# Kernel optimization log

Hardware: AMD Instinct MI355X
Metric: run time of the kernel (lower is better)

## Reference

```python
import jax, jax.numpy as jnp
import numpy as np


def _local_indices(H, W, K):
    # KxK local window per pixel; border neighbors clamped to the image (replicate padding)
    half = K // 2
    d = np.arange(-half, half + 1)
    r = np.clip(np.arange(H)[:, None, None, None] + d[None, None, :, None], 0, H - 1)
    c = np.clip(np.arange(W)[None, :, None, None] + d[None, None, None, :], 0, W - 1)
    return (r * W + c).reshape(H * W, K * K).astype(np.int32)


def setup_inputs():
    B, C, H, W = 2, 32, 128, 128
    K, S = 25, 1024
    N = H * W
    k1, k2, k3, k4 = jax.random.split(jax.random.key(0), 4)
    key_feat = jax.random.normal(k1, (B, C, H, W), dtype=jnp.float32)
    query_feat = jax.random.normal(k2, (B, C, H, W), dtype=jnp.float32)
    segment_target = jax.random.randint(k3, (B, 1, H, W), 0, 64, dtype=jnp.int32)
    local = jnp.broadcast_to(jnp.asarray(_local_indices(H, W, K))[None], (B, N, K * K))
    rand_glob = jax.random.randint(k4, (B, N, S - K * K), 0, N, dtype=jnp.int32)
    sample_inds = jnp.concatenate([local, rand_glob], axis=-1)  # [B, N, S]
    return {"key_feat": key_feat, "query_feat": query_feat,
            "segment_target": segment_target, "sample_inds": sample_inds}


def _affinity_logits(key_f, query_f, sample_inds, chunk=1024):
    # key_f, query_f: [B, N, C]; sample_inds: [B, N, S]
    B, N, C = key_f.shape
    S = sample_inds.shape[-1]
    nchunks = N // chunk
    q_c = query_f.reshape(B, nchunks, chunk, C).transpose(1, 0, 2, 3)
    i_c = sample_inds.reshape(B, nchunks, chunk, S).transpose(1, 0, 2, 3)

    def body(carry, args):
        q, idx = args                                   # [B, chunk, C], [B, chunk, S]
        kg = jax.vmap(lambda kb, ib: kb[ib])(key_f, idx)  # [B, chunk, S, C]
        return carry, jnp.einsum('bnsc,bnc->bns', kg, q)

    _, lc = jax.lax.scan(body, None, (q_c, i_c))        # [nchunks, B, chunk, S]
    logits = lc.transpose(1, 0, 2, 3).reshape(B, N, S)
    return logits * (C ** -0.5)


def _loss(logits, sample_inds, segment_target):
    B, N, S = logits.shape
    seg = segment_target.reshape(B, N)
    samples = jax.vmap(lambda s, i: s[i])(seg, sample_inds)      # [B, N, S]
    targets = (seg[:, :, None] == samples).astype(logits.dtype)
    mask = (seg != 0).astype(logits.dtype)[:, :, None]           # [B, N, 1]
    # weighted_softmax(logits, mask)
    xe = jnp.exp(logits - jnp.max(logits, -1, keepdims=True))
    denom = jnp.sum(xe * mask, -1, keepdims=True)
    y_prob = xe * mask / (denom + 1e-9)
    y_pred = jnp.log(jnp.clip(y_prob, 1e-8, None))
    y_true = targets / (jnp.sum(targets, -1, keepdims=True) + 1e-9)
    # F.kl_div(y_pred, y_true, reduction='none') with 0*log(0) = 0
    kl = jnp.where(y_true > 0,
                   y_true * (jnp.log(jnp.clip(y_true, 1e-30, None)) - y_pred),
                   0.0) * mask
    agg_mask = (jnp.sum(mask, -1) > 0).astype(logits.dtype)
    return jnp.sum(kl) / (jnp.sum(agg_mask) + 1e-9)


def reference(key_feat, query_feat, segment_target, sample_inds):
    B, C, H, W = key_feat.shape
    N = H * W
    key_f = key_feat.reshape(B, C, N).transpose(0, 2, 1)    # [B, N, C]
    query_f = query_feat.reshape(B, C, N).transpose(0, 2, 1)
    logits = _affinity_logits(key_f, query_f, sample_inds)  # [B, N, S], scaled by C**-0.5
    loss = _loss(logits, sample_inds, segment_target)
    return (logits, loss)
```

## Files before the change

### kernel.cpp

```cpp
#include <hip/hip_runtime.h>
#include <stdint.h>

typedef _Float16 h2 __attribute__((ext_vector_type(2)));

static constexpr int CDIM = 32;
static constexpr int NPIX = 16384;
static constexpr int SSAM = 1024;
static constexpr int ROWS_PER_BLOCK = 16;

__device__ __forceinline__ uint16_t f2h(float f) {
    union { _Float16 h; uint16_t u; } c;
    c.h = (_Float16)f;
    return c.u;
}

template<int CTRL>
__device__ __forceinline__ float dpp_add(float x) {
    int y = __builtin_amdgcn_mov_dpp(__float_as_int(x), CTRL, 0xF, 0xF, true);
    return x + __int_as_float(y);
}

__device__ __forceinline__ float dot2(h2 a, h2 b, float c) {
    return __builtin_amdgcn_fdot2(a, b, c, false);
}

__global__ __launch_bounds__(256)
void prep_kernel(const float* __restrict__ key_f,
                 const float* __restrict__ query_f,
                 const int* __restrict__ seg32,
                 uint8_t* __restrict__ key16,
                 uint8_t* __restrict__ q16,
                 uint8_t* __restrict__ seg8,
                 int N, int rows, float scale)
{
    int gI = blockIdx.x * 256 + threadIdx.x;
    if (gI >= rows) return;
    int b = gI / N, n = gI - b * N;
    const size_t cb = (size_t)b * CDIM;

    uint32_t kp[16], qp[16];
#pragma unroll
    for (int c = 0; c < CDIM; c += 2) {
        float k0 = key_f[(cb + c) * N + n];
        float k1 = key_f[(cb + c + 1) * N + n];
        float q0 = query_f[(cb + c) * N + n] * scale;
        float q1 = query_f[(cb + c + 1) * N + n] * scale;
        kp[c >> 1] = (uint32_t)f2h(k0) | ((uint32_t)f2h(k1) << 16);
        qp[c >> 1] = (uint32_t)f2h(q0) | ((uint32_t)f2h(q1) << 16);
    }
    uint4* ko = (uint4*)(key16 + ((size_t)gI << 6));
    uint4* qo = (uint4*)(q16 + ((size_t)gI << 6));
#pragma unroll
    for (int j = 0; j < 4; ++j) {
        ko[j] = make_uint4(kp[4*j], kp[4*j+1], kp[4*j+2], kp[4*j+3]);
        qo[j] = make_uint4(qp[4*j], qp[4*j+1], qp[4*j+2], qp[4*j+3]);
    }
    seg8[gI] = (uint8_t)seg32[gI];
}

__global__ __launch_bounds__(256)
void affinity_multi(const int* __restrict__ inds,
                    const uint8_t* __restrict__ key16,
                    const uint8_t* __restrict__ q16,
                    const uint8_t* __restrict__ seg8,
                    float* __restrict__ out,
                    float* __restrict__ ws_kl)
{
    const int tid  = threadIdx.x;
    const int row0 = blockIdx.x * ROWS_PER_BLOCK;
    const int b    = row0 >> 14;
    const int lane = tid & 63;
    const int w    = tid >> 6;
    const int g    = lane >> 2;
    const int sub  = lane & 3;

    __shared__ __align__(16) uint8_t seg_lds[NPIX];
    __shared__ __align__(16) int     idx_lds[2][SSAM];
    __shared__ float red[2][3][4];

    const uint8_t* sbg = seg8 + ((size_t)b << 14);
#pragma unroll
    for (int r = 0; r < 4; ++r)
        ((uint4*)seg_lds)[(r << 8) + tid] = ((const uint4*)sbg)[(r << 8) + tid];
    ((int4*)idx_lds[0])[tid] = ((const int4*)(inds + ((size_t)row0 << 10)))[tid];
    uint4 qcur = *(const uint4*)(q16 + ((size_t)row0 << 6) + (sub << 4));
    __syncthreads();

    const uint8_t* kb = key16 + ((size_t)b << 20);
    const uint32_t subs = (uint32_t)(sub << 4);
    const int sbase = (w << 8) + g;

    for (int r = 0; r < ROWS_PER_BLOCK; ++r) {
        const int row = row0 + r;
        const int p   = r & 1;
        const int* cur = idx_lds[p];
        const bool hasNext = (r + 1 < ROWS_PER_BLOCK);

        h2 qh0, qh1, qh2, qh3;
        {
            union { uint4 u; h2 h[4]; } qc; qc.u = qcur;
            qh0 = qc.h[0]; qh1 = qc.h[1]; qh2 = qc.h[2]; qh3 = qc.h[3];
        }
        const int seg_n = (int)seg_lds[row & 0x3FFF];

        int idxs[16];
#pragma unroll
        for (int i = 0; i < 16; ++i)
            idxs[i] = cur[sbase + (i << 4)];

        uint4 kd[16];
#pragma unroll
        for (int i = 0; i < 16; ++i)
            kd[i] = *(const uint4*)(kb + (((uint32_t)idxs[i] << 6) | subs));

        int4 pre; uint4 qnext;
        if (hasNext) {
            pre   = ((const int4*)(inds + ((size_t)(row + 1) << 10)))[tid];
            qnext = *(const uint4*)(q16 + ((size_t)(row + 1) << 6) + (sub << 4));
        }
        int tfm = 0;
#pragma unroll
        for (int j = 0; j < 4; ++j) {
            int idx = cur[sbase + (((j << 2) | sub) << 4)];
            if ((int)seg_lds[idx] == seg_n) tfm |= 1 << j;
        }

        float lgo0 = 0.f, lgo1 = 0.f, lgo2 = 0.f, lgo3 = 0.f;
#pragma unroll
        for (int i = 0; i < 16; ++i) {
            union { uint4 u; h2 h[4]; } kc; kc.u = kd[i];
            float acc = dot2(kc.h[0], qh0, 0.f);
            acc = dot2(kc.h[1], qh1, acc);
            acc = dot2(kc.h[2], qh2, acc);
            acc = dot2(kc.h[3], qh3, acc);
            acc = dpp_add<0xB1>(acc);
            acc = dpp_add<0x4E>(acc);
            if (sub == (i & 3)) {
                if ((i >> 2) == 0) lgo0 = acc;
                if ((i >> 2) == 1) lgo1 = acc;
                if ((i >> 2) == 2) lgo2 = acc;
                if ((i >> 2) == 3) lgo3 = acc;
            }
        }

        const size_t rowbase = (size_t)row << 10;
        float* op = out + rowbase + (w << 8) + (sub << 4) + g;
        op[0]   = lgo0;
        op[64]  = lgo1;
        op[128] = lgo2;
        op[192] = lgo3;

        float z  = ((__expf(lgo0) + __expf(lgo1)) + (__expf(lgo2) + __expf(lgo3)));
        float tc = (float)__popc((unsigned)tfm);
        float sl = 0.f;
        sl += (tfm & 1) ? lgo0 : 0.f;
        sl += (tfm & 2) ? lgo1 : 0.f;
        sl += (tfm & 4) ? lgo2 : 0.f;
        sl += (tfm & 8) ? lgo3 : 0.f;

#pragma unroll
        for (int off = 32; off >= 1; off >>= 1) {
            z  += __shfl_xor(z,  off, 64);
            tc += __shfl_xor(tc, off, 64);
            sl += __shfl_xor(sl, off, 64);
        }
        if (lane == 0) {
            red[p][0][w] = z;
            red[p][1][w] = tc;
            red[p][2][w] = sl;
        }
        __syncthreads();

        if (tid == 0) {
            if (seg_n != 0) {
                const float Z  = (red[p][0][0] + red[p][0][1]) + (red[p][0][2] + red[p][0][3]);
                const float T  = (red[p][1][0] + red[p][1][1]) + (red[p][1][2] + red[p][1][3]);
                const float SL = (red[p][2][0] + red[p][2][1]) + (red[p][2][2] + red[p][2][3]);
                ws_kl[row] = -__logf(T) - SL / T + __logf(Z);
            } else {
                ws_kl[row] = 0.f;
            }
        }

        if (hasNext) {
            ((int4*)idx_lds[p ^ 1])[tid] = pre;
            qcur = qnext;
        }
    }
}

__global__ __launch_bounds__(256)
void affinity_fallback(const float* __restrict__ key_f,
                       const float* __restrict__ query_f,
                       const int*   __restrict__ seg32,
                       const int*   __restrict__ inds,
                       float* __restrict__ out,
                       float* __restrict__ ws_kl,
                       int N, int S, float scale)
{
    const int bid = blockIdx.x;
    const int tid = threadIdx.x;
    const int b   = bid / N;

    __shared__ float q_lds[CDIM];
    __shared__ float redA[4], redB[4], redC[4];

    if (tid < CDIM) {
        int n = bid - b * N;
        q_lds[tid] = query_f[((size_t)(b * CDIM + tid)) * N + n];
    }
    const int seg_n = seg32[bid];
    __syncthreads();

    float q[CDIM];
#pragma unroll
    for (int c = 0; c < CDIM; ++c) q[c] = q_lds[c];

    const size_t rowbase = (size_t)bid * S;
    const int4 iv = ((const int4*)(inds + rowbase))[tid];
    const int idxv[4] = {iv.x, iv.y, iv.z, iv.w};

    float lg[4];
    int   tf[4];
#pragma unroll
    for (int k = 0; k < 4; ++k) {
        int idx = idxv[k];
        tf[k] = (seg32[b * N + idx] == seg_n) ? 1 : 0;
        float acc = 0.f;
#pragma unroll
        for (int c = 0; c < CDIM; ++c)
            acc = fmaf(key_f[((size_t)(b * CDIM + c)) * N + idx], q[c], acc);
        lg[k] = acc * scale;
    }
    ((float4*)(out + rowbase))[tid] = make_float4(lg[0], lg[1], lg[2], lg[3]);

    const int lane = tid & 63, wv = tid >> 6;
    float m = fmaxf(fmaxf(lg[0], lg[1]), fmaxf(lg[2], lg[3]));
#pragma unroll
    for (int off = 32; off >= 1; off >>= 1)
        m = fmaxf(m, __shfl_xor(m, off, 64));
    if (lane == 0) redA[wv] = m;
    __syncthreads();
    m = fmaxf(fmaxf(redA[0], redA[1]), fmaxf(redA[2], redA[3]));

    float e[4], z = 0.f, tcnt = 0.f;
#pragma unroll
    for (int k = 0; k < 4; ++k) {
        e[k] = expf(lg[k] - m);
        z += e[k];
        tcnt += (float)tf[k];
    }
#pragma unroll
    for (int off = 32; off >= 1; off >>= 1) {
        z    += __shfl_xor(z, off, 64);
        tcnt += __shfl_xor(tcnt, off, 64);
    }
    if (lane == 0) { redB[wv] = z; redC[wv] = tcnt; }
    __syncthreads();
    const float Z = redB[0] + redB[1] + redB[2] + redB[3];
    const float T = redC[0] + redC[1] + redC[2] + redC[3];

    float kl = 0.f;
    if (seg_n != 0) {
        const float invZ = 1.f / (Z + 1e-9f);
        const float invT = 1.f / (T + 1e-9f);
        const float nlT  = -logf(T + 1e-9f);
#pragma unroll
        for (int k = 0; k < 4; ++k) {
            if (tf[k]) {
                float p = e[k] * invZ;
                float yp = logf(fmaxf(p, 1e-8f));
                kl += invT * (nlT - yp);
            }
        }
    }
#pragma unroll
    for (int off = 32; off >= 1; off >>= 1)
        kl += __shfl_xor(kl, off, 64);
    if (lane == 0) redA[wv] = kl;
    __syncthreads();
    if (tid == 0)
        ws_kl[bid] = redA[0] + redA[1] + redA[2] + redA[3];
}

__global__ __launch_bounds__(1024)
void loss_reduce(const float* __restrict__ ws_kl,
                 const int* __restrict__ seg32,
                 float* __restrict__ out_loss, int rows)
{
    const int tid = threadIdx.x;
    float s = 0.f, c = 0.f;
    for (int i = tid; i < rows; i += 1024) {
        s += ws_kl[i];
        c += (seg32[i] != 0) ? 1.f : 0.f;
    }
#pragma unroll
    for (int off = 32; off >= 1; off >>= 1) {
        s += __shfl_xor(s, off, 64);
        c += __shfl_xor(c, off, 64);
    }
    __shared__ float sA[16], sB[16];
    const int lane = tid & 63, wv = tid >> 6;
    if (lane == 0) { sA[wv] = s; sB[wv] = c; }
    __syncthreads();
    if (tid == 0) {
        float ts = 0.f, tc = 0.f;
#pragma unroll
        for (int k = 0; k < 16; ++k) { ts += sA[k]; tc += sB[k]; }
        out_loss[0] = ts / (tc + 1e-9f);
    }
}

extern "C" void kernel_launch(void* const* d_in, const int* in_sizes, int n_in,
                              void* d_out, int out_size, void* d_ws, size_t ws_size,
                              hipStream_t stream)
{
    const float* key_f   = (const float*)d_in[0];
    const float* query_f = (const float*)d_in[1];
    const int*   seg32   = (const int*)d_in[2];
    const int*   inds    = (const int*)d_in[3];
    float* out = (float*)d_out;

    const int N    = NPIX;
    const int rows = in_sizes[2];
    const int S    = in_sizes[3] / rows;
    const float scale = (float)(1.0 / sqrt((double)CDIM));

    const size_t off_q16 = (size_t)rows * 64;
    const size_t off_s8  = off_q16 + (size_t)rows * 64;
    const size_t off_kl  = (off_s8 + (size_t)rows + 255) & ~(size_t)255;
    const size_t need    = off_kl + (size_t)rows * 4;

    uint8_t* wsb = (uint8_t*)d_ws;
    const bool geom_ok = (S == SSAM) && (rows % N == 0) &&
                         (rows % ROWS_PER_BLOCK == 0);

    if (ws_size >= need && geom_ok) {
        uint8_t* key16 = wsb;
        uint8_t* q16   = wsb + off_q16;
        uint8_t* seg8  = wsb + off_s8;
        float*   wskl  = (float*)(wsb + off_kl);

        prep_kernel<<<(rows + 255) / 256, 256, 0, stream>>>(
            key_f, query_f, seg32, key16, q16, seg8, N, rows, scale);
        affinity_multi<<<rows / ROWS_PER_BLOCK, 256, 0, stream>>>(
            inds, key16, q16, seg8, out, wskl);
        loss_reduce<<<1, 1024, 0, stream>>>(wskl, seg32, out + (size_t)rows * S, rows);
    } else {
        float* wskl = (float*)d_ws;
        affinity_fallback<<<rows, 256, 0, stream>>>(
            key_f, query_f, seg32, inds, out, wskl, N, S, scale);
        loss_reduce<<<1, 1024, 0, stream>>>(wskl, seg32, out + (size_t)rows * S, rows);
    }
}
```

Baseline: 170.3 us.

## Replace per-block segment LDS copy with per-label bitmask rows

Each block used to copy the full 16 KB per-batch segment label array into LDS before any work. The new code builds a bitmask per (batch, label) with atomics and loads only the 2 KB bitmask for the current row's label, double-buffered and prefetched alongside the indices. The target-match test becomes a bit test instead of a byte compare. It also moves the next-row LDS stores ahead of the barrier. The cost is two extra kernel launches (zeroing and bitmask build), atomic contention during the build, and a 2 KB global load per row instead of one 16 KB load per block.

```diff
diff --git a/kernel.cpp b/kernel.cpp
--- a/kernel.cpp
+++ b/kernel.cpp
@@ -25,12 +25,17 @@
 }
 
 __global__ __launch_bounds__(256)
+void zero_words(uint32_t* __restrict__ p, int nwords)
+{
+    int i = blockIdx.x * 256 + threadIdx.x;
+    if (i < nwords) p[i] = 0;
+}
+
+__global__ __launch_bounds__(256)
 void prep_kernel(const float* __restrict__ key_f,
                  const float* __restrict__ query_f,
-                 const int* __restrict__ seg32,
                  uint8_t* __restrict__ key16,
                  uint8_t* __restrict__ q16,
-                 uint8_t* __restrict__ seg8,
                  int N, int rows, float scale)
 {
     int gI = blockIdx.x * 256 + threadIdx.x;
@@ -55,14 +60,26 @@
         ko[j] = make_uint4(kp[4*j], kp[4*j+1], kp[4*j+2], kp[4*j+3]);
         qo[j] = make_uint4(qp[4*j], qp[4*j+1], qp[4*j+2], qp[4*j+3]);
     }
-    seg8[gI] = (uint8_t)seg32[gI];
+}
+
+__global__ __launch_bounds__(256)
+void segbit_build(const int* __restrict__ seg32,
+                  uint32_t* __restrict__ segbit,
+                  int N, int rows)
+{
+    int g = blockIdx.x * 256 + threadIdx.x;
+    if (g >= rows) return;
+    int b = g / N, n = g - b * N;
+    int v = seg32[g] & 63;
+    atomicOr(&segbit[(((size_t)(b * 64 + v)) << 9) + (n >> 5)], 1u << (n & 31));
 }
 
 __global__ __launch_bounds__(256)
 void affinity_multi(const int* __restrict__ inds,
                     const uint8_t* __restrict__ key16,
                     const uint8_t* __restrict__ q16,
-                    const uint8_t* __restrict__ seg8,
+                    const int* __restrict__ seg32,
+                    const uint32_t* __restrict__ segbit,
                     float* __restrict__ out,
                     float* __restrict__ ws_kl)
 {
@@ -74,15 +91,16 @@
     const int g    = lane >> 2;
     const int sub  = lane & 3;
 
-    __shared__ __align__(16) uint8_t seg_lds[NPIX];
-    __shared__ __align__(16) int     idx_lds[2][SSAM];
+    __shared__ __align__(16) int      idx_lds[2][SSAM];
+    __shared__ __align__(16) uint32_t bm_lds[2][512];
     __shared__ float red[2][3][4];
 
-    const uint8_t* sbg = seg8 + ((size_t)b << 14);
-#pragma unroll
-    for (int r = 0; r < 4; ++r)
-        ((uint4*)seg_lds)[(r << 8) + tid] = ((const uint4*)sbg)[(r << 8) + tid];
+    const uint32_t* sbase_bm = segbit + ((size_t)(b * 64) << 9);
+
     ((int4*)idx_lds[0])[tid] = ((const int4*)(inds + ((size_t)row0 << 10)))[tid];
+    int scur = seg32[row0];
+    ((uint2*)bm_lds[0])[tid] =
+        ((const uint2*)(sbase_bm + ((size_t)(scur & 63) << 9)))[tid];
     uint4 qcur = *(const uint4*)(q16 + ((size_t)row0 << 6) + (sub << 4));
     __syncthreads();
 
@@ -101,7 +119,7 @@
             union { uint4 u; h2 h[4]; } qc; qc.u = qcur;
             qh0 = qc.h[0]; qh1 = qc.h[1]; qh2 = qc.h[2]; qh3 = qc.h[3];
         }
-        const int seg_n = (int)seg_lds[row & 0x3FFF];
+        const int seg_n = scur;
 
         int idxs[16];
 #pragma unroll
@@ -113,16 +131,18 @@
         for (int i = 0; i < 16; ++i)
             kd[i] = *(const uint4*)(kb + (((uint32_t)idxs[i] << 6) | subs));
 
-        int4 pre; uint4 qnext;
+        int4 pre; uint4 qnext; uint2 pre_bm; int snext;
         if (hasNext) {
             pre   = ((const int4*)(inds + ((size_t)(row + 1) << 10)))[tid];
             qnext = *(const uint4*)(q16 + ((size_t)(row + 1) << 6) + (sub << 4));
+            snext = seg32[row + 1];
+            pre_bm = ((const uint2*)(sbase_bm + ((size_t)(snext & 63) << 9)))[tid];
         }
         int tfm = 0;
 #pragma unroll
         for (int j = 0; j < 4; ++j) {
             int idx = cur[sbase + (((j << 2) | sub) << 4)];
-            if ((int)seg_lds[idx] == seg_n) tfm |= 1 << j;
+            if ((bm_lds[p][idx >> 5] >> (idx & 31)) & 1u) tfm |= 1 << j;
         }
 
         float lgo0 = 0.f, lgo1 = 0.f, lgo2 = 0.f, lgo3 = 0.f;
@@ -157,7 +177,6 @@
         sl += (tfm & 2) ? lgo1 : 0.f;
         sl += (tfm & 4) ? lgo2 : 0.f;
         sl += (tfm & 8) ? lgo3 : 0.f;
-
 #pragma unroll
         for (int off = 32; off >= 1; off >>= 1) {
             z  += __shfl_xor(z,  off, 64);
@@ -168,6 +187,13 @@
             red[p][0][w] = z;
             red[p][1][w] = tc;
             red[p][2][w] = sl;
+        }
+
+        if (hasNext) {
+            ((int4*)idx_lds[p ^ 1])[tid] = pre;
+            ((uint2*)bm_lds[p ^ 1])[tid] = pre_bm;
+            qcur = qnext;
+            scur = snext;
         }
         __syncthreads();
 
@@ -181,11 +207,6 @@
                 ws_kl[row] = 0.f;
             }
         }
-
-        if (hasNext) {
-            ((int4*)idx_lds[p ^ 1])[tid] = pre;
-            qcur = qnext;
-        }
     }
 }
 
@@ -325,10 +346,12 @@
     const int rows = in_sizes[2];
     const int S    = in_sizes[3] / rows;
     const float scale = (float)(1.0 / sqrt((double)CDIM));
+    const int B    = rows / N;
 
     const size_t off_q16 = (size_t)rows * 64;
-    const size_t off_s8  = off_q16 + (size_t)rows * 64;
-    const size_t off_kl  = (off_s8 + (size_t)rows + 255) & ~(size_t)255;
+    const size_t off_sb  = off_q16 + (size_t)rows * 64;
+    const size_t sb_words = (size_t)B * 64 * 512;
+    const size_t off_kl  = (off_sb + sb_words * 4 + 255) & ~(size_t)255;
     const size_t need    = off_kl + (size_t)rows * 4;
 
     uint8_t* wsb = (uint8_t*)d_ws;
@@ -336,15 +359,19 @@
                          (rows % ROWS_PER_BLOCK == 0);
 
     if (ws_size >= need && geom_ok) {
-        uint8_t* key16 = wsb;
-        uint8_t* q16   = wsb + off_q16;
-        uint8_t* seg8  = wsb + off_s8;
-        float*   wskl  = (float*)(wsb + off_kl);
-
+        uint8_t*  key16  = wsb;
+        uint8_t*  q16    = wsb + off_q16;
+        uint32_t* segbit = (uint32_t*)(wsb + off_sb);
+        float*    wskl   = (float*)(wsb + off_kl);
+
+        zero_words<<<(int)((sb_words + 255) / 256), 256, 0, stream>>>(
+            segbit, (int)sb_words);
         prep_kernel<<<(rows + 255) / 256, 256, 0, stream>>>(
-            key_f, query_f, seg32, key16, q16, seg8, N, rows, scale);
+            key_f, query_f, key16, q16, N, rows, scale);
+        segbit_build<<<(rows + 255) / 256, 256, 0, stream>>>(
+            seg32, segbit, N, rows);
         affinity_multi<<<rows / ROWS_PER_BLOCK, 256, 0, stream>>>(
-            inds, key16, q16, seg8, out, wskl);
+            inds, key16, q16, seg32, segbit, out, wskl);
         loss_reduce<<<1, 1024, 0, stream>>>(wskl, seg32, out + (size_t)rows * S, rows);
     } else {
         float* wskl = (float*)d_ws;
```

Result: slower. 175.2 us (+2.8%).
